# Kernel tuning notes

Measured on AMD Instinct MI355X. Metric: run time of the kernel, lower is better.

Reference implementation:

```python
import jax, jax.numpy as jnp
import numpy as np
from jax import lax

NL = 2        # num mamba layers
D_MODEL = 200
D_STATE = 16
D_CONV = 4
DI = 400      # expand * d_model
DT_RANK = 13  # ceil(d_model / 16)
B = 256
L = 256
EPS = 1e-12


def _ln(x, w, b):
    mu = jnp.mean(x, axis=-1, keepdims=True)
    var = jnp.mean((x - mu) ** 2, axis=-1, keepdims=True)
    return (x - mu) / jnp.sqrt(var + EPS) * w + b


def _mamba(x, in_proj_w, conv_w, conv_b, x_proj_w, dt_proj_w, dt_proj_b, A_log, D, out_proj_w):
    b, l, _ = x.shape
    xz = jnp.einsum('bld,ed->ble', x, in_proj_w)  # [b,l,2*DI]
    xc, z = jnp.split(xz, 2, axis=-1)
    # causal depthwise conv over time (pad d_conv-1 on the left == pytorch pad+slice)
    xt = xc.transpose(0, 2, 1)  # [b,DI,l]
    xt = lax.conv_general_dilated(xt, conv_w[:, None, :], (1,), [(D_CONV - 1, 0)],
                                  dimension_numbers=('NCH', 'OIH', 'NCH'),
                                  feature_group_count=DI)
    xc = jax.nn.silu(xt + conv_b[None, :, None]).transpose(0, 2, 1)  # [b,l,DI]
    x_dbl = jnp.einsum('bld,ed->ble', xc, x_proj_w)  # [b,l,DT_RANK+2*N]
    dt = x_dbl[..., :DT_RANK]
    Bm = x_dbl[..., DT_RANK:DT_RANK + D_STATE]
    Cm = x_dbl[..., DT_RANK + D_STATE:]
    delta = jax.nn.softplus(jnp.einsum('blr,dr->bld', dt, dt_proj_w) + dt_proj_b)  # [b,l,DI]
    A = -jnp.exp(A_log)  # [DI,N]

    def step(h, inp):
        d_t, u_t, B_t, C_t = inp  # [b,DI],[b,DI],[b,N],[b,N]
        dA = jnp.exp(d_t[..., None] * A)  # [b,DI,N]
        h = dA * h + (d_t * u_t)[..., None] * B_t[:, None, :]
        y = jnp.einsum('bdn,bn->bd', h, C_t)
        return h, y

    h0 = jnp.zeros((b, DI, D_STATE), dtype=x.dtype)
    xs = (delta.transpose(1, 0, 2), xc.transpose(1, 0, 2),
          Bm.transpose(1, 0, 2), Cm.transpose(1, 0, 2))
    _, ys = lax.scan(step, h0, xs)
    y = ys.transpose(1, 0, 2) + xc * D  # [b,l,DI]
    y = y * jax.nn.silu(z)
    return jnp.einsum('bld,ed->ble', y, out_proj_w)


def _forward(item_emb, in_proj_w, conv_w, conv_b, x_proj_w, dt_proj_w, dt_proj_b,
             A_log, D, out_proj_w, ln1_w, ln1_b, ffn_w1, ffn_b1, ffn_w2, ffn_b2,
             ffn_ln_w, ffn_ln_b):
    h = item_emb
    for i in range(NL):
        m = _mamba(h, in_proj_w[i], conv_w[i], conv_b[i], x_proj_w[i],
                   dt_proj_w[i], dt_proj_b[i], A_log[i], D[i], out_proj_w[i])
        h = _ln(m + h, ln1_w[i], ln1_b[i])  # num_layers > 1 -> residual branch
        f = jnp.einsum('bld,ed->ble', h, ffn_w1[i]) + ffn_b1[i]
        f = jax.nn.gelu(f, approximate=False)  # torch nn.GELU default = exact
        f = jnp.einsum('ble,de->bld', f, ffn_w2[i]) + ffn_b2[i]
        h = _ln(f + h, ffn_ln_w[i], ffn_ln_b[i])
    c = h[:, -1:, :]
    x_n = h[:, :-1, :]
    return c, x_n


def setup_inputs() -> dict:
    key = jax.random.key(0)
    ks = jax.random.split(key, 10)
    s = 0.02
    f32 = jnp.float32
    A_log = jnp.broadcast_to(jnp.log(jnp.arange(1, D_STATE + 1, dtype=f32)),
                             (NL, DI, D_STATE))
    return {
        'item_emb': jax.random.normal(ks[0], (B, L, D_MODEL), f32),
        'item_seq_len': jax.random.randint(ks[1], (B,), 1, L, jnp.int32),
        'in_proj_w': s * jax.random.normal(ks[2], (NL, 2 * DI, D_MODEL), f32),
        'conv_w': s * jax.random.normal(ks[3], (NL, DI, D_CONV), f32),
        'conv_b': jnp.zeros((NL, DI), f32),
        'x_proj_w': s * jax.random.normal(ks[4], (NL, DT_RANK + 2 * D_STATE, DI), f32),
        'dt_proj_w': s * jax.random.normal(ks[5], (NL, DI, DT_RANK), f32),
        'dt_proj_b': s * jax.random.normal(ks[6], (NL, DI), f32),
        'A_log': A_log,
        'D': jnp.ones((NL, DI), f32),
        'out_proj_w': s * jax.random.normal(ks[7], (NL, D_MODEL, DI), f32),
        'ln1_w': jnp.ones((NL, D_MODEL), f32),
        'ln1_b': jnp.zeros((NL, D_MODEL), f32),
        'ffn_w1': s * jax.random.normal(ks[8], (NL, 4 * D_MODEL, D_MODEL), f32),
        'ffn_b1': jnp.zeros((NL, 4 * D_MODEL), f32),
        'ffn_w2': s * jax.random.normal(ks[9], (NL, D_MODEL, 4 * D_MODEL), f32),
        'ffn_b2': jnp.zeros((NL, D_MODEL), f32),
        'ffn_ln_w': jnp.ones((NL, D_MODEL), f32),
        'ffn_ln_b': jnp.zeros((NL, D_MODEL), f32),
    }


def reference(item_emb, item_seq_len, in_proj_w, conv_w, conv_b, x_proj_w,
              dt_proj_w, dt_proj_b, A_log, D, out_proj_w, ln1_w, ln1_b,
              ffn_w1, ffn_b1, ffn_w2, ffn_b2, ffn_ln_w, ffn_ln_b):
    # item_seq_len is accepted but unused by Mamba4Rec.forward
    return _forward(item_emb, in_proj_w, conv_w, conv_b, x_proj_w, dt_proj_w,
                    dt_proj_b, A_log, D, out_proj_w, ln1_w, ln1_b, ffn_w1,
                    ffn_b1, ffn_w2, ffn_b2, ffn_ln_w, ffn_ln_b)
```

## Files before the change

kernel.cpp:

```cpp
#include <hip/hip_runtime.h>
#include <hip/hip_bf16.h>

#define DM 200
#define DIE 400
#define LSEQ 256
#define NB 256

typedef __hip_bfloat16 bf16;
typedef const float* fp;
typedef __attribute__((ext_vector_type(8))) short short8;
typedef __attribute__((ext_vector_type(4))) short short4_t;
typedef __attribute__((ext_vector_type(4))) float f32x4;

__device__ __forceinline__ float b2f(bf16 x) { return __bfloat162float(x); }
__device__ __forceinline__ bf16  f2b(float x) { return __float2bfloat16(x); }

__device__ __forceinline__ unsigned short f2bbits(float f) {
    union { float f; unsigned int u; } c; c.f = f;
    unsigned int u = c.u;
    unsigned int r = (u + 0x7fffu + ((u >> 16) & 1u)) >> 16;
    return (unsigned short)r;
}
__device__ __forceinline__ void stf(float* p, float v) { *p = v; }
__device__ __forceinline__ void stf(bf16* p, float v) { *p = f2b(v); }

#define W_XP_OFF 320000
#define W_OP_OFF 356000
#define W_F1_OFF 516000
#define W_F2_OFF 836000
#define W_TOTAL  1156000
#define W_BYTES  2312000

__global__ __launch_bounds__(256) void wcvt_kernel(fp a0, fp a1, fp a2, fp a3, fp a4,
                                                   bf16* __restrict__ dst) {
    int g = blockIdx.x * 256 + threadIdx.x;
    if (g >= W_TOTAL / 4) return;
    int idx = g * 4;
    const float* src;
    int off;
    if (idx < W_XP_OFF)      { src = a0; off = idx; }
    else if (idx < W_OP_OFF) { src = a1; off = idx - W_XP_OFF; }
    else if (idx < W_F1_OFF) { src = a2; off = idx - W_OP_OFF; }
    else if (idx < W_F2_OFF) { src = a3; off = idx - W_F1_OFF; }
    else                     { src = a4; off = idx - W_F2_OFF; }
    float4 v = *(const float4*)(src + off);
    short4_t o;
    o.x = (short)f2bbits(v.x); o.y = (short)f2bbits(v.y);
    o.z = (short)f2bbits(v.z); o.w = (short)f2bbits(v.w);
    *(short4_t*)((short*)dst + idx) = o;
}

__global__ __launch_bounds__(256) void cvt_kernel(const float* __restrict__ src,
                                                  bf16* __restrict__ dst, int n4) {
    int g = blockIdx.x * 256 + threadIdx.x;
    if (g >= n4) return;
    int idx = g * 4;
    float4 v = *(const float4*)(src + idx);
    short4_t o;
    o.x = (short)f2bbits(v.x); o.y = (short)f2bbits(v.y);
    o.z = (short)f2bbits(v.z); o.w = (short)f2bbits(v.w);
    *(short4_t*)((short*)dst + idx) = o;
}

template <typename TC, int EPI>
__global__ __launch_bounds__(256) void gemm_mfma(const bf16* __restrict__ A, int lda,
                                                 const bf16* __restrict__ W,
                                                 const float* __restrict__ bias,
                                                 TC* __restrict__ C, int ldc,
                                                 int N, int K) {
    constexpr int LS = 40;
    __shared__ short As[128 * LS];
    __shared__ short Bs[128 * LS];
    const int m0 = blockIdx.x * 128;
    const int n0 = blockIdx.y * 128;
    const int tid = threadIdx.x;
    const int wave = tid >> 6;
    const int lane = tid & 63;
    const int wm = (wave & 1) * 64;
    const int wn = (wave >> 1) * 64;
    const int fm = lane & 15;
    const int quad = lane >> 4;

    f32x4 acc[4][4] = {};

    const int sr = tid >> 1;
    const int sc = (tid & 1) * 16;

    for (int k0 = 0; k0 < K; k0 += 32) {
        {
            const short* src = (const short*)A + (size_t)(m0 + sr) * lda + k0 + sc;
            short* dst = As + sr * LS + sc;
            if (k0 + sc + 16 <= K) {
                *(short8*)dst = *(const short8*)src;
                *(short8*)(dst + 8) = *(const short8*)(src + 8);
            } else {
#pragma unroll
                for (int j = 0; j < 16; ++j)
                    dst[j] = (k0 + sc + j < K) ? src[j] : (short)0;
            }
        }
        {
            short* dst = Bs + sr * LS + sc;
            if (n0 + sr < N) {
                const short* src = (const short*)W + (size_t)(n0 + sr) * K + k0 + sc;
                if (k0 + sc + 16 <= K) {
                    *(short8*)dst = *(const short8*)src;
                    *(short8*)(dst + 8) = *(const short8*)(src + 8);
                } else {
#pragma unroll
                    for (int j = 0; j < 16; ++j)
                        dst[j] = (k0 + sc + j < K) ? src[j] : (short)0;
                }
            } else {
#pragma unroll
                for (int j = 0; j < 16; ++j) dst[j] = 0;
            }
        }
        __syncthreads();
        short8 af[4], bfr[4];
#pragma unroll
        for (int i = 0; i < 4; ++i)
            af[i] = *(const short8*)(As + (wm + i * 16 + fm) * LS + quad * 8);
#pragma unroll
        for (int j = 0; j < 4; ++j)
            bfr[j] = *(const short8*)(Bs + (wn + j * 16 + fm) * LS + quad * 8);
#pragma unroll
        for (int i = 0; i < 4; ++i)
#pragma unroll
            for (int j = 0; j < 4; ++j)
                acc[i][j] = __builtin_amdgcn_mfma_f32_16x16x32_bf16(af[i], bfr[j], acc[i][j], 0, 0, 0);
        __syncthreads();
    }

#pragma unroll
    for (int j = 0; j < 4; ++j) {
        int n = n0 + wn + j * 16 + fm;
        if (n >= N) continue;
        float bv = (EPI == 2 || EPI == 3) ? bias[n] : 0.f;
#pragma unroll
        for (int i = 0; i < 4; ++i) {
#pragma unroll
            for (int r = 0; r < 4; ++r) {
                int m = m0 + wm + i * 16 + quad * 4 + r;
                float v = acc[i][j][r];
                if (EPI == 2) {
                    v += bv;
                    v = 0.5f * v * (1.f + erff(v * 0.70710678118654752f));
                } else if (EPI == 3) {
                    v += bv;
                }
                stf(&C[(size_t)m * ldc + n], v);
            }
        }
    }
}

__global__ __launch_bounds__(256) void conv_silu_inplace(bf16* __restrict__ xz,
                                                         const float* __restrict__ cw,
                                                         const float* __restrict__ cb,
                                                         int total ) {
    int idx = blockIdx.x * 256 + threadIdx.x;
    if (idx >= total) return;
    int d = idx % DIE;
    int b = idx / DIE;
    float w0 = cw[d * 4 + 0];
    float w1 = cw[d * 4 + 1];
    float w2 = cw[d * 4 + 2];
    float w3 = cw[d * 4 + 3];
    float bias = cb[d];
    float x0 = 0.f, x1 = 0.f, x2 = 0.f;
    bf16* p = xz + (size_t)b * LSEQ * 800 + d;
    for (int t = 0; t < LSEQ; ++t) {
        float x = b2f(*p);
        float s = bias + w0 * x0 + w1 * x1 + w2 * x2 + w3 * x;
        x0 = x1; x1 = x2; x2 = x;
        float sig = __builtin_amdgcn_rcpf(1.f + __expf(-s));
        *p = f2b(s * sig);
        p += 800;
    }
}

template <bool FAST>
__device__ __forceinline__ void scan_body(const float* __restrict__ rp,
                                          bf16* __restrict__ xp,
                                          const float* Wr, const float* A2,
                                          float bdt, float Dv) {
    float h[16];
#pragma unroll
    for (int n = 0; n < 16; ++n) h[n] = 0.f;

    auto scan_step = [&](const float* cur, float ut, float zv, bf16* outp) {
        float dtv = bdt;
#pragma unroll
        for (int r = 0; r < 13; ++r) dtv += Wr[r] * cur[r];
        float sp = (dtv > 20.f) ? dtv : __logf(1.f + __expf(dtv));
        float du = sp * ut;
        float dA[16];
        if (FAST) {
            float r1 = __expf(-sp);
            float r2 = r1 * r1, r3 = r2 * r1, r4 = r2 * r2;
            float r5 = r4 * r1, r6 = r4 * r2, r7 = r4 * r3, r8 = r4 * r4;
            dA[0] = r1;  dA[1] = r2;  dA[2] = r3;  dA[3] = r4;
            dA[4] = r5;  dA[5] = r6;  dA[6] = r7;  dA[7] = r8;
            dA[8] = r8 * r1;  dA[9] = r8 * r2;  dA[10] = r8 * r3;  dA[11] = r8 * r4;
            dA[12] = r8 * r5; dA[13] = r8 * r6; dA[14] = r8 * r7;  dA[15] = r8 * r8;
        } else {
#pragma unroll
            for (int n = 0; n < 16; ++n) dA[n] = __expf(sp * A2[n]);
        }
        float yv = 0.f;
#pragma unroll
        for (int n = 0; n < 16; ++n) {
            h[n] = dA[n] * h[n] + du * cur[13 + n];
            yv += h[n] * cur[29 + n];
        }
        yv += ut * Dv;
        float sig = __builtin_amdgcn_rcpf(1.f + __expf(-zv));
        *outp = f2b(yv * zv * sig);
    };

    float ca[45], cbuf[45];
#pragma unroll
    for (int j = 0; j < 45; ++j) ca[j] = rp[j];
    float utA = b2f(xp[0]);
    float zvA = b2f(xp[400]);

    for (int t = 0; t < LSEQ; t += 2) {
#pragma unroll
        for (int j = 0; j < 45; ++j) cbuf[j] = rp[45 + j];
        float utB = b2f(xp[800]);
        float zvB = b2f(xp[1200]);

        scan_step(ca, utA, zvA, xp);

        if (t + 2 < LSEQ) {
#pragma unroll
            for (int j = 0; j < 45; ++j) ca[j] = rp[90 + j];
            utA = b2f(xp[1600]);
            zvA = b2f(xp[2000]);
        }

        scan_step(cbuf, utB, zvB, xp + 800);

        rp += 90;
        xp += 1600;
    }
}

__global__ __launch_bounds__(256) void scan_kernel(const float* __restrict__ xdbl,
                                                   bf16* __restrict__ xz,
                                                   const float* __restrict__ dt_w,
                                                   const float* __restrict__ dt_b,
                                                   const float* __restrict__ A_log,
                                                   const float* __restrict__ Dw) {
    const int b = blockIdx.x >> 1;
    const int half = blockIdx.x & 1;
    const int tid = threadIdx.x;
    if (tid >= 200) return;
    const int d = half * 200 + tid;

    float A2[16], Wr[13];
    bool fast = true;
#pragma unroll
    for (int n = 0; n < 16; ++n) {
        A2[n] = -__expf(A_log[d * 16 + n]);
        fast = fast && (fabsf(A2[n] + (float)(n + 1)) < 1e-3f);
    }
#pragma unroll
    for (int r = 0; r < 13; ++r) Wr[r] = dt_w[d * 13 + r];
    const float bdt = dt_b[d];
    const float Dv = Dw[d];

    const float* __restrict__ rp = xdbl + (size_t)b * LSEQ * 45;
    bf16* __restrict__ xp = xz + (size_t)b * LSEQ * 800 + d;

    if (fast) scan_body<true>(rp, xp, Wr, A2, bdt, Dv);
    else      scan_body<false>(rp, xp, Wr, A2, bdt, Dv);
}

__global__ __launch_bounds__(256) void ln_res_kernel(const float* __restrict__ xa,
                                                     const float* xb,
                                                     const float* __restrict__ w,
                                                     const float* __restrict__ bias,
                                                     float* dst,
                                                     bf16* __restrict__ dstb, int rows) {
    int wave = threadIdx.x >> 6;
    int lane = threadIdx.x & 63;
    int row = blockIdx.x * 4 + wave;
    if (row >= rows) return;
    const float* pa = xa + (size_t)row * DM;
    const float* pb = xb + (size_t)row * DM;
    float v[4];
    float sum = 0.f, sq = 0.f;
#pragma unroll
    for (int i = 0; i < 4; ++i) {
        int c = lane + i * 64;
        float t = 0.f;
        if (c < DM) t = pa[c] + pb[c];
        v[i] = t;
        sum += t;
        sq += t * t;
    }
#pragma unroll
    for (int off = 32; off > 0; off >>= 1) {
        sum += __shfl_down(sum, off);
        sq += __shfl_down(sq, off);
    }
    sum = __shfl(sum, 0);
    sq = __shfl(sq, 0);
    float mu = sum * (1.f / DM);
    float var = fmaxf(sq * (1.f / DM) - mu * mu, 0.f);
    float rstd = rsqrtf(var + 1e-12f);
    float* pd = dst + (size_t)row * DM;
    bf16* pdb = dstb + (size_t)row * DM;
#pragma unroll
    for (int i = 0; i < 4; ++i) {
        int c = lane + i * 64;
        if (c < DM) {
            float o = (v[i] - mu) * rstd * w[c] + bias[c];
            pd[c] = o;
            pdb[c] = f2b(o);
        }
    }
}

__global__ __launch_bounds__(256) void write_out_kernel(const float* __restrict__ h,
                                                        float* __restrict__ out,
                                                        int b0, int total ) {
    int idx = blockIdx.x * 256 + threadIdx.x;
    if (idx >= total) return;
    int d = idx % DM;
    int bl = idx / DM;
    int l = bl % LSEQ;
    int b = b0 + bl / LSEQ;
    float v = h[idx];
    if (l == LSEQ - 1) {
        out[b * DM + d] = v;
    } else {
        out[(size_t)NB * DM + ((size_t)(b * (LSEQ - 1) + l) * DM + d)] = v;
    }
}

extern "C" void kernel_launch(void* const* d_in, const int* in_sizes, int n_in,
                              void* d_out, int out_size, void* d_ws, size_t ws_size,
                              hipStream_t stream) {
    fp emb       = (fp)d_in[0];
    fp in_proj_w = (fp)d_in[2];
    fp conv_w    = (fp)d_in[3];
    fp conv_b    = (fp)d_in[4];
    fp x_proj_w  = (fp)d_in[5];
    fp dt_proj_w = (fp)d_in[6];
    fp dt_proj_b = (fp)d_in[7];
    fp A_log     = (fp)d_in[8];
    fp Dw        = (fp)d_in[9];
    fp out_proj_w= (fp)d_in[10];
    fp ln1_w     = (fp)d_in[11];
    fp ln1_b     = (fp)d_in[12];
    fp ffn_w1    = (fp)d_in[13];
    fp ffn_b1    = (fp)d_in[14];
    fp ffn_w2    = (fp)d_in[15];
    fp ffn_b2    = (fp)d_in[16];
    fp ffn_ln_w  = (fp)d_in[17];
    fp ffn_ln_b  = (fp)d_in[18];

    const int cands[8] = {256, 128, 64, 32, 16, 8, 4, 2};
    int cb = 2;
    for (int ci = 0; ci < 8; ++ci) {
        size_t rcx = (size_t)cands[ci] * LSEQ;
        if (rcx * 3780 + W_BYTES + 1024 <= ws_size) { cb = cands[ci]; break; }
    }
    const size_t rc = (size_t)cb * LSEQ;

    bf16*  wb   = (bf16*)d_ws;
    bf16*  xz   = (bf16*)((char*)d_ws + W_BYTES);
    bf16*  hb   = xz + rc * 800;
    float* xdbl = (float*)(hb + rc * 200);
    float* m    = xdbl + rc * 45;
    float* h    = m + rc * 200;

    wcvt_kernel<<<(W_TOTAL / 4 + 255) / 256, 256, 0, stream>>>(
        in_proj_w, x_proj_w, out_proj_w, ffn_w1, ffn_w2, wb);

    const int rcDM = (int)rc * DM;
    const int gm = (int)rc / 128;

    for (int b0 = 0; b0 < NB; b0 += cb) {
        const float* emb_chunk = emb + (size_t)b0 * LSEQ * DM;

        cvt_kernel<<<(rcDM / 4 + 255) / 256, 256, 0, stream>>>(emb_chunk, hb, rcDM / 4);

        for (int i = 0; i < 2; ++i) {
            const bf16* wb_in = wb + (size_t)i * 160000;
            const bf16* wb_xp = wb + W_XP_OFF + (size_t)i * 18000;
            const bf16* wb_op = wb + W_OP_OFF + (size_t)i * 80000;
            const bf16* wb_f1 = wb + W_F1_OFF + (size_t)i * 160000;
            const bf16* wb_f2 = wb + W_F2_OFF + (size_t)i * 160000;
            fp cw    = conv_w + (size_t)i * 400 * 4;
            fp cbp   = conv_b + (size_t)i * 400;
            fp w_dt  = dt_proj_w + (size_t)i * 400 * 13;
            fp b_dt  = dt_proj_b + (size_t)i * 400;
            fp Ai    = A_log + (size_t)i * 400 * 16;
            fp Di    = Dw + (size_t)i * 400;
            fp l1w   = ln1_w + (size_t)i * 200;
            fp l1b   = ln1_b + (size_t)i * 200;
            fp f1b   = ffn_b1 + (size_t)i * 800;
            fp f2b_  = ffn_b2 + (size_t)i * 200;
            fp flw   = ffn_ln_w + (size_t)i * 200;
            fp flb   = ffn_ln_b + (size_t)i * 200;

            const float* hin = (i == 0) ? emb_chunk : h;

            gemm_mfma<bf16, 0><<<dim3(gm, 7), 256, 0, stream>>>(
                hb, 200, wb_in, nullptr, xz, 800, 800, 200);
            conv_silu_inplace<<<(cb * DIE + 255) / 256, 256, 0, stream>>>(xz, cw, cbp, cb * DIE);
            gemm_mfma<float, 0><<<dim3(gm, 1), 256, 0, stream>>>(
                xz, 800, wb_xp, nullptr, xdbl, 45, 45, 400);
            scan_kernel<<<cb * 2, 256, 0, stream>>>(xdbl, xz, w_dt, b_dt, Ai, Di);
            gemm_mfma<float, 0><<<dim3(gm, 2), 256, 0, stream>>>(
                xz, 800, wb_op, nullptr, m, 200, 200, 400);
            ln_res_kernel<<<rc / 4, 256, 0, stream>>>(m, hin, l1w, l1b, h, hb, (int)rc);
            gemm_mfma<bf16, 2><<<dim3(gm, 7), 256, 0, stream>>>(
                hb, 200, wb_f1, f1b, xz, 800, 800, 200);
            gemm_mfma<float, 3><<<dim3(gm, 2), 256, 0, stream>>>(
                xz, 800, wb_f2, f2b_, m, 200, 200, 800);
            ln_res_kernel<<<rc / 4, 256, 0, stream>>>(m, h, flw, flb, h, hb, (int)rc);
        }

        write_out_kernel<<<rcDM / 256, 256, 0, stream>>>(h, (float*)d_out, b0, rcDM);
    }
}
```

Before: 1.306 ms.

## Hoist dt projection and softplus out of scan into MFMA GEMM

```diff
diff --git a/kernel.cpp b/kernel.cpp
--- a/kernel.cpp
+++ b/kernel.cpp
@@ -28,10 +28,11 @@
 #define W_OP_OFF 356000
 #define W_F1_OFF 516000
 #define W_F2_OFF 836000
-#define W_TOTAL  1156000
-#define W_BYTES  2312000
-
-__global__ __launch_bounds__(256) void wcvt_kernel(fp a0, fp a1, fp a2, fp a3, fp a4,
+#define W_DT_OFF 1156000
+#define W_TOTAL  1166400
+#define W_BYTES  2332800
+
+__global__ __launch_bounds__(256) void wcvt_kernel(fp a0, fp a1, fp a2, fp a3, fp a4, fp a5,
                                                    bf16* __restrict__ dst) {
     int g = blockIdx.x * 256 + threadIdx.x;
     if (g >= W_TOTAL / 4) return;
@@ -42,7 +43,8 @@
     else if (idx < W_OP_OFF) { src = a1; off = idx - W_XP_OFF; }
     else if (idx < W_F1_OFF) { src = a2; off = idx - W_OP_OFF; }
     else if (idx < W_F2_OFF) { src = a3; off = idx - W_F1_OFF; }
-    else                     { src = a4; off = idx - W_F2_OFF; }
+    else if (idx < W_DT_OFF) { src = a4; off = idx - W_F2_OFF; }
+    else                     { src = a5; off = idx - W_DT_OFF; }
     float4 v = *(const float4*)(src + off);
     short4_t o;
     o.x = (short)f2bbits(v.x); o.y = (short)f2bbits(v.y);
@@ -67,6 +69,7 @@
                                                  const bf16* __restrict__ W,
                                                  const float* __restrict__ bias,
                                                  TC* __restrict__ C, int ldc,
+                                                 bf16* __restrict__ C2, int ldc2,
                                                  int N, int K) {
     constexpr int LS = 40;
     __shared__ short As[128 * LS];
@@ -136,7 +139,7 @@
     for (int j = 0; j < 4; ++j) {
         int n = n0 + wn + j * 16 + fm;
         if (n >= N) continue;
-        float bv = (EPI == 2 || EPI == 3) ? bias[n] : 0.f;
+        float bv = (EPI == 2 || EPI == 3 || EPI == 4) ? bias[n] : 0.f;
 #pragma unroll
         for (int i = 0; i < 4; ++i) {
 #pragma unroll
@@ -148,8 +151,14 @@
                     v = 0.5f * v * (1.f + erff(v * 0.70710678118654752f));
                 } else if (EPI == 3) {
                     v += bv;
+                } else if (EPI == 4) {
+                    v += bv;
+                    v = (v > 20.f) ? v : __logf(1.f + __expf(v));
+                } else if (EPI == 5) {
+                    if (n >= 400) v = v * __builtin_amdgcn_rcpf(1.f + __expf(-v));
                 }
                 stf(&C[(size_t)m * ldc + n], v);
+                if (EPI == 6 && n < 13) C2[(size_t)m * ldc2 + n] = f2b(v);
             }
         }
     }
@@ -181,21 +190,21 @@
 }
 
 template <bool FAST>
-__device__ __forceinline__ void scan_body(const float* __restrict__ rp,
-                                          bf16* __restrict__ xp,
-                                          const float* Wr, const float* A2,
-                                          float bdt, float Dv) {
+__device__ __forceinline__ void scan_body2(const float* __restrict__ rp,
+                                           const float* __restrict__ spp,
+                                           bf16* __restrict__ xp,
+                                           const float* A2, float Dv) {
     float h[16];
 #pragma unroll
     for (int n = 0; n < 16; ++n) h[n] = 0.f;
 
-    auto scan_step = [&](const float* cur, float ut, float zv, bf16* outp) {
-        float dtv = bdt;
-#pragma unroll
-        for (int r = 0; r < 13; ++r) dtv += Wr[r] * cur[r];
-        float sp = (dtv > 20.f) ? dtv : __logf(1.f + __expf(dtv));
-        float du = sp * ut;
-        float dA[16];
+    auto precomp = [&](int o45, int osp, int ox,
+                       float* Bb, float* Cb, float* dA, float& du, float& ut, float& zs) {
+#pragma unroll
+        for (int j = 0; j < 16; ++j) { Bb[j] = rp[o45 + 13 + j]; Cb[j] = rp[o45 + 29 + j]; }
+        float sp = spp[osp];
+        ut = b2f(xp[ox]);
+        zs = b2f(xp[ox + 400]);
         if (FAST) {
             float r1 = __expf(-sp);
             float r2 = r1 * r1, r3 = r2 * r1, r4 = r2 * r2;
@@ -208,49 +217,42 @@
 #pragma unroll
             for (int n = 0; n < 16; ++n) dA[n] = __expf(sp * A2[n]);
         }
-        float yv = 0.f;
-#pragma unroll
-        for (int n = 0; n < 16; ++n) {
-            h[n] = dA[n] * h[n] + du * cur[13 + n];
-            yv += h[n] * cur[29 + n];
-        }
-        yv += ut * Dv;
-        float sig = __builtin_amdgcn_rcpf(1.f + __expf(-zv));
-        *outp = f2b(yv * zv * sig);
+        du = sp * ut;
     };
-
-    float ca[45], cbuf[45];
-#pragma unroll
-    for (int j = 0; j < 45; ++j) ca[j] = rp[j];
-    float utA = b2f(xp[0]);
-    float zvA = b2f(xp[400]);
+    auto compute = [&](const float* Bb, const float* Cb, const float* dA,
+                       float du, float ut, float zs, int ox) {
+#pragma unroll
+        for (int n = 0; n < 16; ++n) h[n] = dA[n] * h[n] + du * Bb[n];
+        float y0 = 0.f, y1 = 0.f, y2 = 0.f, y3 = 0.f;
+#pragma unroll
+        for (int n = 0; n < 4; ++n) {
+            y0 += h[n] * Cb[n];
+            y1 += h[4 + n] * Cb[4 + n];
+            y2 += h[8 + n] * Cb[8 + n];
+            y3 += h[12 + n] * Cb[12 + n];
+        }
+        float yv = (y0 + y1) + (y2 + y3) + ut * Dv;
+        xp[ox] = f2b(yv * zs);
+    };
+
+    float BA[16], CA[16], dAA[16], BB[16], CB[16], dAB[16];
+    float duA, utA, zsA, duB, utB, zsB;
+
+    precomp(0, 0, 0, BA, CA, dAA, duA, utA, zsA);
 
     for (int t = 0; t < LSEQ; t += 2) {
-#pragma unroll
-        for (int j = 0; j < 45; ++j) cbuf[j] = rp[45 + j];
-        float utB = b2f(xp[800]);
-        float zvB = b2f(xp[1200]);
-
-        scan_step(ca, utA, zvA, xp);
-
-        if (t + 2 < LSEQ) {
-#pragma unroll
-            for (int j = 0; j < 45; ++j) ca[j] = rp[90 + j];
-            utA = b2f(xp[1600]);
-            zvA = b2f(xp[2000]);
-        }
-
-        scan_step(cbuf, utB, zvB, xp + 800);
-
-        rp += 90;
-        xp += 1600;
+        precomp(45, 400, 800, BB, CB, dAB, duB, utB, zsB);
+        compute(BA, CA, dAA, duA, utA, zsA, 0);
+        if (t + 2 < LSEQ)
+            precomp(90, 800, 1600, BA, CA, dAA, duA, utA, zsA);
+        compute(BB, CB, dAB, duB, utB, zsB, 800);
+        rp += 90; spp += 800; xp += 1600;
     }
 }
 
 __global__ __launch_bounds__(256) void scan_kernel(const float* __restrict__ xdbl,
+                                                   const float* __restrict__ spbuf,
                                                    bf16* __restrict__ xz,
-                                                   const float* __restrict__ dt_w,
-                                                   const float* __restrict__ dt_b,
                                                    const float* __restrict__ A_log,
                                                    const float* __restrict__ Dw) {
     const int b = blockIdx.x >> 1;
@@ -259,23 +261,21 @@
     if (tid >= 200) return;
     const int d = half * 200 + tid;
 
-    float A2[16], Wr[13];
+    float A2[16];
     bool fast = true;
 #pragma unroll
     for (int n = 0; n < 16; ++n) {
         A2[n] = -__expf(A_log[d * 16 + n]);
         fast = fast && (fabsf(A2[n] + (float)(n + 1)) < 1e-3f);
     }
-#pragma unroll
-    for (int r = 0; r < 13; ++r) Wr[r] = dt_w[d * 13 + r];
-    const float bdt = dt_b[d];
     const float Dv = Dw[d];
 
-    const float* __restrict__ rp = xdbl + (size_t)b * LSEQ * 45;
+    const float* __restrict__ rp  = xdbl + (size_t)b * LSEQ * 45;
+    const float* __restrict__ spp = spbuf + (size_t)b * LSEQ * 400 + d;
     bf16* __restrict__ xp = xz + (size_t)b * LSEQ * 800 + d;
 
-    if (fast) scan_body<true>(rp, xp, Wr, A2, bdt, Dv);
-    else      scan_body<false>(rp, xp, Wr, A2, bdt, Dv);
+    if (fast) scan_body2<true>(rp, spp, xp, A2, Dv);
+    else      scan_body2<false>(rp, spp, xp, A2, Dv);
 }
 
 __global__ __launch_bounds__(256) void ln_res_kernel(const float* __restrict__ xa,
@@ -367,19 +367,21 @@
     int cb = 2;
     for (int ci = 0; ci < 8; ++ci) {
         size_t rcx = (size_t)cands[ci] * LSEQ;
-        if (rcx * 3780 + W_BYTES + 1024 <= ws_size) { cb = cands[ci]; break; }
+        if (rcx * 5412 + W_BYTES + 1024 <= ws_size) { cb = cands[ci]; break; }
     }
     const size_t rc = (size_t)cb * LSEQ;
 
-    bf16*  wb   = (bf16*)d_ws;
-    bf16*  xz   = (bf16*)((char*)d_ws + W_BYTES);
-    bf16*  hb   = xz + rc * 800;
-    float* xdbl = (float*)(hb + rc * 200);
-    float* m    = xdbl + rc * 45;
-    float* h    = m + rc * 200;
+    bf16*  wb    = (bf16*)d_ws;
+    bf16*  xz    = (bf16*)((char*)d_ws + W_BYTES);
+    bf16*  hb    = xz + rc * 800;
+    bf16*  dtb   = hb + rc * 200;
+    float* spbuf = (float*)(dtb + rc * 16);
+    float* xdbl  = spbuf + rc * 400;
+    float* m     = xdbl + rc * 45;
+    float* h     = m + rc * 200;
 
     wcvt_kernel<<<(W_TOTAL / 4 + 255) / 256, 256, 0, stream>>>(
-        in_proj_w, x_proj_w, out_proj_w, ffn_w1, ffn_w2, wb);
+        in_proj_w, x_proj_w, out_proj_w, ffn_w1, ffn_w2, dt_proj_w, wb);
 
     const int rcDM = (int)rc * DM;
     const int gm = (int)rc / 128;
@@ -395,9 +397,9 @@
             const bf16* wb_op = wb + W_OP_OFF + (size_t)i * 80000;
             const bf16* wb_f1 = wb + W_F1_OFF + (size_t)i * 160000;
             const bf16* wb_f2 = wb + W_F2_OFF + (size_t)i * 160000;
+            const bf16* wb_dt = wb + W_DT_OFF + (size_t)i * 5200;
             fp cw    = conv_w + (size_t)i * 400 * 4;
             fp cbp   = conv_b + (size_t)i * 400;
-            fp w_dt  = dt_proj_w + (size_t)i * 400 * 13;
             fp b_dt  = dt_proj_b + (size_t)i * 400;
             fp Ai    = A_log + (size_t)i * 400 * 16;
             fp Di    = Dw + (size_t)i * 400;
@@ -410,19 +412,21 @@
 
             const float* hin = (i == 0) ? emb_chunk : h;
 
-            gemm_mfma<bf16, 0><<<dim3(gm, 7), 256, 0, stream>>>(
-                hb, 200, wb_in, nullptr, xz, 800, 800, 200);
+            gemm_mfma<bf16, 5><<<dim3(gm, 7), 256, 0, stream>>>(
+                hb, 200, wb_in, nullptr, xz, 800, nullptr, 0, 800, 200);
             conv_silu_inplace<<<(cb * DIE + 255) / 256, 256, 0, stream>>>(xz, cw, cbp, cb * DIE);
-            gemm_mfma<float, 0><<<dim3(gm, 1), 256, 0, stream>>>(
-                xz, 800, wb_xp, nullptr, xdbl, 45, 45, 400);
-            scan_kernel<<<cb * 2, 256, 0, stream>>>(xdbl, xz, w_dt, b_dt, Ai, Di);
+            gemm_mfma<float, 6><<<dim3(gm, 1), 256, 0, stream>>>(
+                xz, 800, wb_xp, nullptr, xdbl, 45, dtb, 16, 45, 400);
+            gemm_mfma<float, 4><<<dim3(gm, 4), 256, 0, stream>>>(
+                dtb, 16, wb_dt, b_dt, spbuf, 400, nullptr, 0, 400, 13);
+            scan_kernel<<<cb * 2, 256, 0, stream>>>(xdbl, spbuf, xz, Ai, Di);
             gemm_mfma<float, 0><<<dim3(gm, 2), 256, 0, stream>>>(
-                xz, 800, wb_op, nullptr, m, 200, 200, 400);
+                xz, 800, wb_op, nullptr, m, 200, nullptr, 0, 200, 400);
             ln_res_kernel<<<rc / 4, 256, 0, stream>>>(m, hin, l1w, l1b, h, hb, (int)rc);
             gemm_mfma<bf16, 2><<<dim3(gm, 7), 256, 0, stream>>>(
-                hb, 200, wb_f1, f1b, xz, 800, 800, 200);
+                hb, 200, wb_f1, f1b, xz, 800, nullptr, 0, 800, 200);
             gemm_mfma<float, 3><<<dim3(gm, 2), 256, 0, stream>>>(
-                xz, 800, wb_f2, f2b_, m, 200, 200, 800);
+                xz, 800, wb_f2, f2b_, m, 200, nullptr, 0, 200, 800);
             ln_res_kernel<<<rc / 4, 256, 0, stream>>>(m, h, flw, flb, h, hb, (int)rc);
         }
 
```

Result: slower. 1.515 ms (+16.0%).

## Fuse z-gate SiLU into in_proj GEMM, restructure scan prefetch, fuse output write

Applied to the files above, without the earlier changes.

```diff
diff --git a/kernel.cpp b/kernel.cpp
--- a/kernel.cpp
+++ b/kernel.cpp
@@ -148,6 +148,8 @@
                     v = 0.5f * v * (1.f + erff(v * 0.70710678118654752f));
                 } else if (EPI == 3) {
                     v += bv;
+                } else if (EPI == 5) {
+                    if (n >= 400) v = v * __builtin_amdgcn_rcpf(1.f + __expf(-v));
                 }
                 stf(&C[(size_t)m * ldc + n], v);
             }
@@ -189,13 +191,16 @@
 #pragma unroll
     for (int n = 0; n < 16; ++n) h[n] = 0.f;
 
-    auto scan_step = [&](const float* cur, float ut, float zv, bf16* outp) {
+    auto precomp = [&](int o45, int ox,
+                       float* Bb, float* Cb, float* dA, float& du, float& ut, float& zs) {
         float dtv = bdt;
 #pragma unroll
-        for (int r = 0; r < 13; ++r) dtv += Wr[r] * cur[r];
+        for (int r = 0; r < 13; ++r) dtv += Wr[r] * rp[o45 + r];
+#pragma unroll
+        for (int j = 0; j < 16; ++j) { Bb[j] = rp[o45 + 13 + j]; Cb[j] = rp[o45 + 29 + j]; }
+        ut = b2f(xp[ox]);
+        zs = b2f(xp[ox + 400]);
         float sp = (dtv > 20.f) ? dtv : __logf(1.f + __expf(dtv));
-        float du = sp * ut;
-        float dA[16];
         if (FAST) {
             float r1 = __expf(-sp);
             float r2 = r1 * r1, r3 = r2 * r1, r4 = r2 * r2;
@@ -208,42 +213,36 @@
 #pragma unroll
             for (int n = 0; n < 16; ++n) dA[n] = __expf(sp * A2[n]);
         }
-        float yv = 0.f;
-#pragma unroll
-        for (int n = 0; n < 16; ++n) {
-            h[n] = dA[n] * h[n] + du * cur[13 + n];
-            yv += h[n] * cur[29 + n];
-        }
-        yv += ut * Dv;
-        float sig = __builtin_amdgcn_rcpf(1.f + __expf(-zv));
-        *outp = f2b(yv * zv * sig);
+        du = sp * ut;
     };
-
-    float ca[45], cbuf[45];
-#pragma unroll
-    for (int j = 0; j < 45; ++j) ca[j] = rp[j];
-    float utA = b2f(xp[0]);
-    float zvA = b2f(xp[400]);
+    auto compute = [&](const float* Bb, const float* Cb, const float* dA,
+                       float du, float ut, float zs, int ox) {
+#pragma unroll
+        for (int n = 0; n < 16; ++n) h[n] = dA[n] * h[n] + du * Bb[n];
+        float y0 = 0.f, y1 = 0.f, y2 = 0.f, y3 = 0.f;
+#pragma unroll
+        for (int n = 0; n < 4; ++n) {
+            y0 += h[n] * Cb[n];
+            y1 += h[4 + n] * Cb[4 + n];
+            y2 += h[8 + n] * Cb[8 + n];
+            y3 += h[12 + n] * Cb[12 + n];
+        }
+        float yv = (y0 + y1) + (y2 + y3) + ut * Dv;
+        xp[ox] = f2b(yv * zs);
+    };
+
+    float BA[16], CA[16], dAA[16], BB[16], CB[16], dAB[16];
+    float duA, utA, zsA, duB, utB, zsB;
+
+    precomp(0, 0, BA, CA, dAA, duA, utA, zsA);
 
     for (int t = 0; t < LSEQ; t += 2) {
-#pragma unroll
-        for (int j = 0; j < 45; ++j) cbuf[j] = rp[45 + j];
-        float utB = b2f(xp[800]);
-        float zvB = b2f(xp[1200]);
-
-        scan_step(ca, utA, zvA, xp);
-
-        if (t + 2 < LSEQ) {
-#pragma unroll
-            for (int j = 0; j < 45; ++j) ca[j] = rp[90 + j];
-            utA = b2f(xp[1600]);
-            zvA = b2f(xp[2000]);
-        }
-
-        scan_step(cbuf, utB, zvB, xp + 800);
-
-        rp += 90;
-        xp += 1600;
+        precomp(45, 800, BB, CB, dAB, duB, utB, zsB);
+        compute(BA, CA, dAA, duA, utA, zsA, 0);
+        if (t + 2 < LSEQ)
+            precomp(90, 1600, BA, CA, dAA, duA, utA, zsA);
+        compute(BB, CB, dAB, duB, utB, zsB, 800);
+        rp += 90; xp += 1600;
     }
 }
 
@@ -283,7 +282,8 @@
                                                      const float* __restrict__ w,
                                                      const float* __restrict__ bias,
                                                      float* dst,
-                                                     bf16* __restrict__ dstb, int rows) {
+                                                     bf16* __restrict__ dstb, int rows,
+                                                     float* __restrict__ outp, int b0) {
     int wave = threadIdx.x >> 6;
     int lane = threadIdx.x & 63;
     int row = blockIdx.x * 4 + wave;
@@ -311,33 +311,29 @@
     float mu = sum * (1.f / DM);
     float var = fmaxf(sq * (1.f / DM) - mu * mu, 0.f);
     float rstd = rsqrtf(var + 1e-12f);
-    float* pd = dst + (size_t)row * DM;
-    bf16* pdb = dstb + (size_t)row * DM;
-#pragma unroll
-    for (int i = 0; i < 4; ++i) {
-        int c = lane + i * 64;
-        if (c < DM) {
-            float o = (v[i] - mu) * rstd * w[c] + bias[c];
-            pd[c] = o;
-            pdb[c] = f2b(o);
-        }
-    }
-}
-
-__global__ __launch_bounds__(256) void write_out_kernel(const float* __restrict__ h,
-                                                        float* __restrict__ out,
-                                                        int b0, int total ) {
-    int idx = blockIdx.x * 256 + threadIdx.x;
-    if (idx >= total) return;
-    int d = idx % DM;
-    int bl = idx / DM;
-    int l = bl % LSEQ;
-    int b = b0 + bl / LSEQ;
-    float v = h[idx];
-    if (l == LSEQ - 1) {
-        out[b * DM + d] = v;
+    if (outp) {
+        int bb = b0 + row / LSEQ;
+        int l = row % LSEQ;
+        float* po = (l == LSEQ - 1)
+                        ? outp + (size_t)bb * DM
+                        : outp + (size_t)NB * DM + (size_t)(bb * (LSEQ - 1) + l) * DM;
+#pragma unroll
+        for (int i = 0; i < 4; ++i) {
+            int c = lane + i * 64;
+            if (c < DM) po[c] = (v[i] - mu) * rstd * w[c] + bias[c];
+        }
     } else {
-        out[(size_t)NB * DM + ((size_t)(b * (LSEQ - 1) + l) * DM + d)] = v;
+        float* pd = dst + (size_t)row * DM;
+        bf16* pdb = dstb + (size_t)row * DM;
+#pragma unroll
+        for (int i = 0; i < 4; ++i) {
+            int c = lane + i * 64;
+            if (c < DM) {
+                float o = (v[i] - mu) * rstd * w[c] + bias[c];
+                pd[c] = o;
+                pdb[c] = f2b(o);
+            }
+        }
     }
 }
 
@@ -409,8 +405,9 @@
             fp flb   = ffn_ln_b + (size_t)i * 200;
 
             const float* hin = (i == 0) ? emb_chunk : h;
-
-            gemm_mfma<bf16, 0><<<dim3(gm, 7), 256, 0, stream>>>(
+            const bool last = (i == 1);
+
+            gemm_mfma<bf16, 5><<<dim3(gm, 7), 256, 0, stream>>>(
                 hb, 200, wb_in, nullptr, xz, 800, 800, 200);
             conv_silu_inplace<<<(cb * DIE + 255) / 256, 256, 0, stream>>>(xz, cw, cbp, cb * DIE);
             gemm_mfma<float, 0><<<dim3(gm, 1), 256, 0, stream>>>(
@@ -418,14 +415,14 @@
             scan_kernel<<<cb * 2, 256, 0, stream>>>(xdbl, xz, w_dt, b_dt, Ai, Di);
             gemm_mfma<float, 0><<<dim3(gm, 2), 256, 0, stream>>>(
                 xz, 800, wb_op, nullptr, m, 200, 200, 400);
-            ln_res_kernel<<<rc / 4, 256, 0, stream>>>(m, hin, l1w, l1b, h, hb, (int)rc);
+            ln_res_kernel<<<rc / 4, 256, 0, stream>>>(m, hin, l1w, l1b, h, hb, (int)rc,
+                                                      nullptr, 0);
             gemm_mfma<bf16, 2><<<dim3(gm, 7), 256, 0, stream>>>(
                 hb, 200, wb_f1, f1b, xz, 800, 800, 200);
             gemm_mfma<float, 3><<<dim3(gm, 2), 256, 0, stream>>>(
                 xz, 800, wb_f2, f2b_, m, 200, 200, 800);
-            ln_res_kernel<<<rc / 4, 256, 0, stream>>>(m, h, flw, flb, h, hb, (int)rc);
-        }
-
-        write_out_kernel<<<rcDM / 256, 256, 0, stream>>>(h, (float*)d_out, b0, rcDM);
-    }
-}
+            ln_res_kernel<<<rc / 4, 256, 0, stream>>>(m, h, flw, flb, h, hb, (int)rc,
+                                                      last ? (float*)d_out : nullptr, b0);
+        }
+    }
+}
```

Measured after the change: 1.311 ms. About the same (+0.3%).
